# Optimization experiments

Hardware: AMD Instinct MI355X
Metric: run time of the kernel (lower is better)

## Reference

```python
import jax, jax.numpy as jnp
import numpy as np

ANCHOR_PX = (32, 64, 96, 128)
FIELD = 16.0
POOL, TILES = 2, 3
TAU, NMS_IOU = 0.5, 0.3
MAX_DET = 512
HF, WF, DF = 128, 128, 512
HIDDEN = 1024


def _create_anchors():
    # anchors centered on the field grid, rows ordered (i, j, k): x,y = upper-left, w=h=size
    ii, jj, kk = np.meshgrid(np.arange(HF), np.arange(WF), np.arange(len(ANCHOR_PX)), indexing='ij')
    sz = np.asarray(ANCHOR_PX, np.float32)[kk]
    x = jj * FIELD + FIELD / 2 - sz / 2
    y = ii * FIELD + FIELD / 2 - sz / 2
    return np.stack([x.ravel(), y.ravel(), sz.ravel(), sz.ravel()], axis=1).astype(np.float32)


def setup_inputs() -> dict:
    key = jax.random.key(0)
    ks = jax.random.split(key, 8)
    return {
        'features': jax.random.normal(ks[0], (HF, WF, DF), jnp.float32),
        'rpn_obj': jax.random.normal(ks[1], (HF, WF, 2 * len(ANCHOR_PX)), jnp.float32),
        'rpn_reg': 0.1 * jax.random.normal(ks[2], (HF, WF, 4 * len(ANCHOR_PX)), jnp.float32),
        'anchors': jnp.asarray(_create_anchors()),
        'W1': 0.02 * jax.random.normal(ks[3], (TILES * TILES * DF, HIDDEN), jnp.float32),
        'b1': jnp.zeros((HIDDEN,), jnp.float32),
        'W2': 0.02 * jax.random.normal(ks[4], (HIDDEN, HIDDEN), jnp.float32),
        'b2': jnp.zeros((HIDDEN,), jnp.float32),
        'W3': 0.02 * jax.random.normal(ks[5], (HIDDEN, 4), jnp.float32),
        'b3': jnp.zeros((4,), jnp.float32),
    }


def _map_outputs(output, anchors):
    # faithful port of map_outputs: 3D RPN tensor -> per-anchor rows via gather
    K = len(ANCHOR_PX)
    ap = jnp.asarray(ANCHOR_PX, jnp.float32)
    idx = jnp.argmax(anchors[:, 3:4] == ap[None, :], axis=1).astype(jnp.int32)
    px = ((anchors[:, 0] + anchors[:, 2] / 2) / FIELD).astype(jnp.int32)
    py = ((anchors[:, 1] + anchors[:, 3] / 2) / FIELD).astype(jnp.int32)
    H, W, D = output.shape
    reshaped = output.reshape(H, W, K, D // K)
    return reshaped[py, px, idx]  # (Na, D//K)


def _unparameterize(reg, anchors):
    acx = anchors[:, 0] + anchors[:, 2] / 2
    acy = anchors[:, 1] + anchors[:, 3] / 2
    cx = acx + reg[:, 0] * anchors[:, 2]
    cy = acy + reg[:, 1] * anchors[:, 3]
    w = anchors[:, 2] * jnp.exp(reg[:, 2])
    h = anchors[:, 3] * jnp.exp(reg[:, 3])
    return jnp.stack([cx - w / 2, cy - h / 2, w, h], axis=1)


def _iou_matrix(boxes):
    x1, y1 = boxes[:, 0], boxes[:, 1]
    x2, y2 = x1 + boxes[:, 2], y1 + boxes[:, 3]
    ix = jnp.maximum(0.0, jnp.minimum(x2[:, None], x2[None, :]) - jnp.maximum(x1[:, None], x1[None, :]))
    iy = jnp.maximum(0.0, jnp.minimum(y2[:, None], y2[None, :]) - jnp.maximum(y1[:, None], y1[None, :]))
    inter = ix * iy
    area = boxes[:, 2] * boxes[:, 3]
    return inter / (area[:, None] + area[None, :] - inter + 1e-8)


def _nms_keep(iou, valid, thr):
    # greedy NMS on score-sorted boxes: sequential scan over rows
    n = valid.shape[0]
    rng = jnp.arange(n)
    def step(keep, i):
        suppressed = jnp.any((iou[i] > thr) & keep & (rng < i))
        k = valid[i] & jnp.logical_not(suppressed)
        return keep.at[i].set(k), k
    keep, _ = jax.lax.scan(step, jnp.zeros((n,), bool), rng)
    return keep


def _roialign(features, boxes):
    # pool x pool bilinear samples per tile, tiles x tiles tiles per box, max-pooled per tile
    M = boxes.shape[0]
    T = TILES * POOL
    t = (jnp.arange(T, dtype=jnp.float32) + 0.5) / T
    fx = (boxes[:, 0:1] + t[None, :] * boxes[:, 2:3]) / FIELD - 0.5  # (M, T)
    fy = (boxes[:, 1:2] + t[None, :] * boxes[:, 3:4]) / FIELD - 0.5
    def grid(c, n):
        c = jnp.clip(c, 0.0, n - 1.0)
        c0 = jnp.floor(c).astype(jnp.int32)
        c1 = jnp.minimum(c0 + 1, n - 1)
        return c0, c1, c - c0
    x0, x1, wx = grid(fx, WF)
    y0, y1, wy = grid(fy, HF)
    def g(yi, xi):
        return features[yi[:, :, None], xi[:, None, :]]  # (M, T, T, D)
    wy0, wy1 = (1 - wy)[:, :, None, None], wy[:, :, None, None]
    wx0, wx1 = (1 - wx)[:, None, :, None], wx[:, None, :, None]
    val = g(y0, x0) * wy0 * wx0 + g(y0, x1) * wy0 * wx1 + g(y1, x0) * wy1 * wx0 + g(y1, x1) * wy1 * wx1
    val = val.reshape(M, TILES, POOL, TILES, POOL, DF)
    return jnp.max(val, axis=(2, 4))  # (M, TILES, TILES, D)


def reference(features, rpn_obj, rpn_reg, anchors, W1, b1, W2, b2, W3, b3):
    obj = _map_outputs(rpn_obj, anchors)            # (Na, 2)
    reg = _map_outputs(rpn_reg, anchors)            # (Na, 4)
    scores = jax.nn.softmax(obj, axis=1)[:, 1]      # objectness
    boxes = _unparameterize(reg, anchors)           # proposals (Na, 4)
    # threshold + top-k (fixed-shape surrogate for boolean_mask)
    masked = jnp.where(scores > TAU, scores, -jnp.inf)
    top_scores, top_idx = jax.lax.top_k(masked, MAX_DET)
    valid = jnp.isfinite(top_scores)
    sel = boxes[top_idx]                            # (MAX_DET, 4)
    keep = _nms_keep(_iou_matrix(sel), valid, NMS_IOU)
    # roialign + fast-rcnn refinement head
    pooled = _roialign(features, sel).reshape(MAX_DET, -1)
    h = jax.nn.relu(pooled @ W1 + b1)
    h = jax.nn.relu(h @ W2 + b2)
    deltas = h @ W3 + b3
    refined = _unparameterize(deltas, sel)
    sc = jnp.where(valid, top_scores, 0.0)
    out = jnp.concatenate([refined, sc[:, None]], axis=1)
    return out * keep[:, None].astype(out.dtype)    # (MAX_DET, 5)
```

## Files before the change

kernel.cpp:

```cpp
#include <hip/hip_runtime.h>
#include <math.h>

#define HFD 128
#define WFD 128
#define DFD 512
#define KA  4
#define NA  (HFD*WFD*KA)
#define MAXD 512
#define HID 1024
#define FIN 4608
#define CMAX 2048
#define NBUCK 1025
#define BINCAP 64
#define TAUF 0.5f
#define NMS_THR 0.3f
#define SPLITK 8

typedef __bf16 bf16x8 __attribute__((ext_vector_type(8)));
typedef float  floatx4 __attribute__((ext_vector_type(4)));

__device__ __forceinline__ unsigned short f2bf(float x) {
    unsigned u = __float_as_uint(x);
    unsigned r = (u + 0x7FFFu + ((u >> 16) & 1u)) >> 16;
    return (unsigned short)r;
}

__global__ void init_kernel(unsigned* __restrict__ hist) {
    int t = threadIdx.x;
    for (int i = t; i < NBUCK; i += 1024) hist[i] = 0u;
}

__global__ __launch_bounds__(256)
void front_kernel(const float* __restrict__ rpn_obj,
                  unsigned* __restrict__ hist,
                  unsigned long long* __restrict__ bins,
                  const float* __restrict__ W1,
                  unsigned short* __restrict__ W1t,
                  const float* __restrict__ W2,
                  unsigned short* __restrict__ W2t) {
    __shared__ float tile[32][33];
    int b = blockIdx.x;
    if (b < 256) {
        int n = b * 256 + threadIdx.x;
        float2 o = ((const float2*)rpn_obj)[n];
        float m  = fmaxf(o.x, o.y);
        float e0 = expf(o.x - m), e1 = expf(o.y - m);
        float s  = e1 / (e0 + e1);
        if (s > TAUF) {
            unsigned bits = __float_as_uint(s);
            unsigned bk = (bits - 0x3F000000u) >> 13;
            unsigned slot = atomicAdd(&hist[bk], 1u);
            if (slot < BINCAP)
                bins[bk * BINCAP + slot] =
                    ((unsigned long long)bits << 32) |
                    (unsigned long long)(~(unsigned)n);
        }
        return;
    }
    b -= 256;
    const float* W; unsigned short* Wt; int K, N;
    if (b < (FIN / 32) * (HID / 32)) { W = W1; Wt = W1t; K = FIN; N = HID; }
    else { b -= (FIN / 32) * (HID / 32); W = W2; Wt = W2t; K = HID; N = HID; }
    int bn = (b & (N / 32 - 1)) * 32;
    int bk = (b / (N / 32)) * 32;
    int tx = threadIdx.x & 31, ty = threadIdx.x >> 5;
#pragma unroll
    for (int r = 0; r < 32; r += 8)
        tile[ty + r][tx] = W[(long)(bk + ty + r) * N + bn + tx];
    __syncthreads();
#pragma unroll
    for (int r = 0; r < 32; r += 8)
        Wt[(long)(bn + ty + r) * K + bk + tx] = f2bf(tile[tx][ty + r]);
}

__global__ __launch_bounds__(1024)
void tgs_kernel(const unsigned* __restrict__ hist,
                const unsigned long long* __restrict__ bins,
                const float* __restrict__ rpn_reg,
                const float* __restrict__ anchors,
                float* __restrict__ sel,
                float* __restrict__ top_score,
                unsigned* __restrict__ valid_g) {
    __shared__ unsigned long long keys[CMAX];
    __shared__ unsigned Hs[NBUCK];
    __shared__ unsigned Ssc[1024];
    __shared__ unsigned cntS;
    __shared__ unsigned thrS;

    int tid = threadIdx.x;
    int wave = tid >> 6, lane = tid & 63;

    if (tid == 0) cntS = 0u;
    for (int i = tid; i < NBUCK; i += 1024) Hs[i] = hist[i];
    __syncthreads();
    unsigned sv = Hs[tid + 1];
    Ssc[tid] = sv;
    __syncthreads();
    for (int d = 1; d < 1024; d <<= 1) {
        unsigned add = (tid + d < 1024) ? Ssc[tid + d] : 0u;
        __syncthreads();
        Ssc[tid] += add;
        __syncthreads();
    }
    if (tid == 0 && Ssc[0] < MAXD) thrS = 0u;
    {
        unsigned Scur = Ssc[tid];
        unsigned Snxt = (tid == 1023) ? 0u : Ssc[tid + 1];
        if (Scur >= MAXD && Snxt < MAXD) thrS = (unsigned)(tid + 1);
    }
    __syncthreads();
    unsigned thr = thrS;

    for (int b = (int)thr + wave; b < NBUCK; b += 16) {
        unsigned c = Hs[b]; if (c > BINCAP) c = BINCAP;
        unsigned base = 0;
        if (lane == 0 && c > 0) base = atomicAdd(&cntS, c);
        base = __shfl(base, 0);
        if (c > 0 && lane < c && base + lane < CMAX)
            keys[base + lane] = bins[(long)b * BINCAP + lane];
    }
    __syncthreads();
    unsigned cnt = cntS; if (cnt > CMAX) cnt = CMAX;
    int SN = (cnt <= 1024) ? 1024 : CMAX;
    for (int i = tid; i < SN; i += 1024)
        if (i >= (int)cnt) keys[i] = 0ULL;
    __syncthreads();

    for (int k = 2; k <= SN; k <<= 1) {
        for (int j = k >> 1; j > 0; j >>= 1) {
            for (int i = tid; i < SN; i += 1024) {
                int ixj = i ^ j;
                if (ixj > i) {
                    unsigned long long a = keys[i], b = keys[ixj];
                    bool up = ((i & k) == 0);
                    if ((a < b) == up) { keys[i] = b; keys[ixj] = a; }
                }
            }
            __syncthreads();
        }
    }

    if (tid < MAXD) {
        unsigned long long e = keys[tid];
        unsigned sbits = (unsigned)(e >> 32);
        bool v = (sbits != 0u);
        unsigned idx = v ? (unsigned)(~(unsigned)e) : 0u;
        int cell = idx >> 2, kk = idx & 3;
        float4 rg = *(const float4*)&rpn_reg[cell * 16 + 4 * kk];
        float4 an = *(const float4*)&anchors[idx * 4];
        float acx = an.x + an.z * 0.5f;
        float acy = an.y + an.w * 0.5f;
        float cx = acx + rg.x * an.z;
        float cy = acy + rg.y * an.w;
        float w  = an.z * expf(rg.z);
        float h  = an.w * expf(rg.w);
        ((float4*)sel)[tid] = make_float4(cx - 0.5f * w, cy - 0.5f * h, w, h);
        top_score[tid] = v ? __uint_as_float(sbits) : 0.0f;
        valid_g[tid]   = v ? 1u : 0u;
    }
}

__global__ __launch_bounds__(512)
void iou_mask_kernel(const float* __restrict__ sel,
                     unsigned long long* __restrict__ mask) {
    int i = blockIdx.x;
    int j = threadIdx.x;
    float4 bi = ((const float4*)sel)[i];
    float4 bj = ((const float4*)sel)[j];
    float x2i = bi.x + bi.z, y2i = bi.y + bi.w;
    float x2j = bj.x + bj.z, y2j = bj.y + bj.w;
    float ai = bi.z * bi.w, aj = bj.z * bj.w;
    float ix = fmaxf(0.0f, fminf(x2i, x2j) - fmaxf(bi.x, bj.x));
    float iy = fmaxf(0.0f, fminf(y2i, y2j) - fmaxf(bi.y, bj.y));
    float inter = ix * iy;
    float iou = inter / (ai + aj - inter + 1e-8f);
    unsigned long long bal = __ballot(iou > NMS_THR);
    if ((j & 63) == 0) mask[i * 8 + (j >> 6)] = bal;
}

__global__ __launch_bounds__(64)
void nms_scan_kernel(const unsigned long long* __restrict__ mask,
                     const unsigned* __restrict__ valid,
                     unsigned* __restrict__ keep) {
    int lane = threadIdx.x;
    unsigned long long w[8][8];
#pragma unroll
    for (int g = 0; g < 8; ++g)
#pragma unroll
        for (int t = 0; t < 8; ++t)
            if (t <= g) w[g][t] = mask[(g * 64 + lane) * 8 + t];
    unsigned long long vb[8];
#pragma unroll
    for (int g = 0; g < 8; ++g)
        vb[g] = __ballot(valid[g * 64 + lane] != 0u);

    unsigned long long keepw[8];
#pragma unroll
    for (int g = 0; g < 8; ++g) {
        bool pre = false;
#pragma unroll
        for (int t = 0; t < 8; ++t)
            if (t < g) pre = pre || ((w[g][t] & keepw[t]) != 0ULL);
        unsigned long long alive = vb[g] & ~__ballot(pre);
        unsigned long long intra = w[g][g];
        unsigned long long kg = 0ULL;
#pragma unroll
        for (int b = 0; b < 64; ++b) {
            unsigned long long sup = __ballot((intra >> b) & 1ULL);
            if ((alive >> b) & 1ULL) {
                kg |= 1ULL << b;
                alive &= ~sup;
            }
        }
        keepw[g] = kg;
        keep[g * 64 + lane] = (unsigned)((kg >> lane) & 1ULL);
    }
}

__global__ __launch_bounds__(256)
void roialign_kernel(const float* __restrict__ feat,
                     const float* __restrict__ sel,
                     unsigned short* __restrict__ pooled) {
    int mrow = blockIdx.x;
    int c = threadIdx.x;
    float4 b = ((const float4*)sel)[mrow];
    float bx = b.x, by = b.y, bw = b.z, bh = b.w;
    float vmax0[9], vmax1[9];
#pragma unroll
    for (int t = 0; t < 9; ++t) { vmax0[t] = -INFINITY; vmax1[t] = -INFINITY; }
#pragma unroll
    for (int p = 0; p < 6; ++p) {
        float fy = (by + ((float)p + 0.5f) / 6.0f * bh) / 16.0f - 0.5f;
        fy = fminf(fmaxf(fy, 0.0f), 127.0f);
        int y0 = (int)floorf(fy);
        int y1 = min(y0 + 1, 127);
        float wy = fy - (float)y0;
#pragma unroll
        for (int q = 0; q < 6; ++q) {
            float fx = (bx + ((float)q + 0.5f) / 6.0f * bw) / 16.0f - 0.5f;
            fx = fminf(fmaxf(fx, 0.0f), 127.0f);
            int x0 = (int)floorf(fx);
            int x1 = min(x0 + 1, 127);
            float wx = fx - (float)x0;
            const float* f00 = feat + (y0 * WFD + x0) * DFD;
            const float* f01 = feat + (y0 * WFD + x1) * DFD;
            const float* f10 = feat + (y1 * WFD + x0) * DFD;
            const float* f11 = feat + (y1 * WFD + x1) * DFD;
            float w00 = (1.0f - wy) * (1.0f - wx);
            float w01 = (1.0f - wy) * wx;
            float w10 = wy * (1.0f - wx);
            float w11 = wy * wx;
            int t = (p >> 1) * 3 + (q >> 1);
            float v0 = f00[c] * w00 + f01[c] * w01 + f10[c] * w10 + f11[c] * w11;
            float v1 = f00[c + 256] * w00 + f01[c + 256] * w01 +
                       f10[c + 256] * w10 + f11[c + 256] * w11;
            vmax0[t] = fmaxf(vmax0[t], v0);
            vmax1[t] = fmaxf(vmax1[t], v1);
        }
    }
#pragma unroll
    for (int t = 0; t < 9; ++t) {
        pooled[mrow * FIN + t * DFD + c] = f2bf(vmax0[t]);
        pooled[mrow * FIN + t * DFD + c + 256] = f2bf(vmax1[t]);
    }
}

#define LDSTRIDE 40
__global__ __launch_bounds__(256)
void mfma_gemm_kernel(const unsigned short* __restrict__ A,
                      const unsigned short* __restrict__ Bt,
                      float* __restrict__ Cpart,
                      int M, int N, int K) {
    __shared__ unsigned short As[64 * LDSTRIDE];
    __shared__ unsigned short Bs[64 * LDSTRIDE];
    int tid = threadIdx.x;
    int wave = tid >> 6, lane = tid & 63;
    int bm = blockIdx.y * 64, bn = blockIdx.x * 64;
    int KC = K / SPLITK;
    int ks = blockIdx.z * KC;

    floatx4 acc[4] = {};
    int lr = tid >> 2;
    int lk = (tid & 3) << 3;
    int frow = lane & 15, quad = lane >> 4;

    const unsigned short* Ap = A + (long)(bm + lr) * K + lk;
    const unsigned short* Bp = Bt + (long)(bn + lr) * K + lk;

    for (int k0 = ks; k0 < ks + KC; k0 += 32) {
        uint4 av = *(const uint4*)(Ap + k0);
        uint4 bv = *(const uint4*)(Bp + k0);
        *(uint4*)&As[lr * LDSTRIDE + lk] = av;
        *(uint4*)&Bs[lr * LDSTRIDE + lk] = bv;
        __syncthreads();
        bf16x8 af = *(const bf16x8*)&As[(wave * 16 + frow) * LDSTRIDE + quad * 8];
#pragma unroll
        for (int t = 0; t < 4; ++t) {
            bf16x8 bfv = *(const bf16x8*)&Bs[(t * 16 + frow) * LDSTRIDE + quad * 8];
            acc[t] = __builtin_amdgcn_mfma_f32_16x16x32_bf16(af, bfv, acc[t], 0, 0, 0);
        }
        __syncthreads();
    }

    float* Cp = Cpart + (long)blockIdx.z * M * N;
#pragma unroll
    for (int t = 0; t < 4; ++t) {
#pragma unroll
        for (int r = 0; r < 4; ++r) {
            int m = bm + wave * 16 + quad * 4 + r;
            int n = bn + t * 16 + frow;
            Cp[(long)m * N + n] = acc[t][r];
        }
    }
}

__global__ __launch_bounds__(256)
void reduce_bias_relu_kernel(const float* __restrict__ Cpart,
                             const float* __restrict__ bias,
                             unsigned short* __restrict__ out_bf,
                             int MN, int N) {
    int i4 = (blockIdx.x * blockDim.x + threadIdx.x) * 4;
    if (i4 >= MN) return;
    float4 s = *(const float4*)&Cpart[i4];
#pragma unroll
    for (int z = 1; z < SPLITK; ++z) {
        float4 p = *(const float4*)&Cpart[(long)z * MN + i4];
        s.x += p.x; s.y += p.y; s.z += p.z; s.w += p.w;
    }
    int n = i4 & (N - 1);
    float4 bi = *(const float4*)&bias[n];
    s.x = fmaxf(s.x + bi.x, 0.0f);
    s.y = fmaxf(s.y + bi.y, 0.0f);
    s.z = fmaxf(s.z + bi.z, 0.0f);
    s.w = fmaxf(s.w + bi.w, 0.0f);
    uint2 o;
    o.x = (unsigned)f2bf(s.x) | ((unsigned)f2bf(s.y) << 16);
    o.y = (unsigned)f2bf(s.z) | ((unsigned)f2bf(s.w) << 16);
    *(uint2*)&out_bf[i4] = o;
}

__global__ __launch_bounds__(256)
void rowhead_kernel(const float* __restrict__ Cpart,
                    const float* __restrict__ b2,
                    const float* __restrict__ W3,
                    const float* __restrict__ b3,
                    const float* __restrict__ sel,
                    const float* __restrict__ top_score,
                    const unsigned* __restrict__ valid,
                    const unsigned* __restrict__ keep,
                    float* __restrict__ out) {
    __shared__ float red[4][4];
    int r = blockIdx.x, t = threadIdx.x;
    int wave = t >> 6, lane = t & 63;
    int c = t * 4;
    const int MN = MAXD * HID;
    float4 s = *(const float4*)&Cpart[(long)r * HID + c];
#pragma unroll
    for (int z = 1; z < SPLITK; ++z) {
        float4 p = *(const float4*)&Cpart[(long)z * MN + (long)r * HID + c];
        s.x += p.x; s.y += p.y; s.z += p.z; s.w += p.w;
    }
    float4 bi = *(const float4*)&b2[c];
    float h[4];
    h[0] = fmaxf(s.x + bi.x, 0.0f);
    h[1] = fmaxf(s.y + bi.y, 0.0f);
    h[2] = fmaxf(s.z + bi.z, 0.0f);
    h[3] = fmaxf(s.w + bi.w, 0.0f);
    float a0 = 0.f, a1 = 0.f, a2 = 0.f, a3 = 0.f;
#pragma unroll
    for (int i = 0; i < 4; ++i) {
        float4 w = *(const float4*)&W3[(c + i) * 4];
        a0 += h[i] * w.x; a1 += h[i] * w.y;
        a2 += h[i] * w.z; a3 += h[i] * w.w;
    }
#pragma unroll
    for (int off = 32; off > 0; off >>= 1) {
        a0 += __shfl_down(a0, off);
        a1 += __shfl_down(a1, off);
        a2 += __shfl_down(a2, off);
        a3 += __shfl_down(a3, off);
    }
    if (lane == 0) {
        red[wave][0] = a0; red[wave][1] = a1;
        red[wave][2] = a2; red[wave][3] = a3;
    }
    __syncthreads();
    if (t == 0) {
        float d0 = red[0][0] + red[1][0] + red[2][0] + red[3][0] + b3[0];
        float d1 = red[0][1] + red[1][1] + red[2][1] + red[3][1] + b3[1];
        float d2 = red[0][2] + red[1][2] + red[2][2] + red[3][2] + b3[2];
        float d3 = red[0][3] + red[1][3] + red[2][3] + red[3][3] + b3[3];
        if (keep[r] != 0u) {
            float4 b = ((const float4*)sel)[r];
            float acx = b.x + 0.5f * b.z;
            float acy = b.y + 0.5f * b.w;
            float cx = acx + d0 * b.z;
            float cy = acy + d1 * b.w;
            float nw = b.z * expf(d2);
            float nh = b.w * expf(d3);
            out[r * 5 + 0] = cx - 0.5f * nw;
            out[r * 5 + 1] = cy - 0.5f * nh;
            out[r * 5 + 2] = nw;
            out[r * 5 + 3] = nh;
            out[r * 5 + 4] = (valid[r] != 0u) ? top_score[r] : 0.0f;
        } else {
            out[r * 5 + 0] = 0.0f;
            out[r * 5 + 1] = 0.0f;
            out[r * 5 + 2] = 0.0f;
            out[r * 5 + 3] = 0.0f;
            out[r * 5 + 4] = 0.0f;
        }
    }
}

extern "C" void kernel_launch(void* const* d_in, const int* in_sizes, int n_in,
                              void* d_out, int out_size, void* d_ws, size_t ws_size,
                              hipStream_t stream) {
    const float* features = (const float*)d_in[0];
    const float* rpn_obj  = (const float*)d_in[1];
    const float* rpn_reg  = (const float*)d_in[2];
    const float* anchors  = (const float*)d_in[3];
    const float* W1 = (const float*)d_in[4];
    const float* b1 = (const float*)d_in[5];
    const float* W2 = (const float*)d_in[6];
    const float* b2 = (const float*)d_in[7];
    const float* W3 = (const float*)d_in[8];
    const float* b3 = (const float*)d_in[9];
    float* out = (float*)d_out;

    char* ws = (char*)d_ws;
    size_t off = 0;
    auto alloc = [&](size_t bytes) {
        char* p = ws + off;
        off += (bytes + 255) & ~(size_t)255;
        return p;
    };
    unsigned* hist      = (unsigned*)alloc(NBUCK * sizeof(unsigned));
    unsigned long long* bins =
        (unsigned long long*)alloc((size_t)NBUCK * BINCAP * 8);
    float*    sel       = (float*)alloc(MAXD * 4 * sizeof(float));
    float*    top_score = (float*)alloc(MAXD * sizeof(float));
    unsigned* valid     = (unsigned*)alloc(MAXD * sizeof(unsigned));
    unsigned* keep      = (unsigned*)alloc(MAXD * sizeof(unsigned));
    unsigned long long* mask = (unsigned long long*)alloc(MAXD * 8 * 8);
    unsigned short* pooled = (unsigned short*)alloc((size_t)MAXD * FIN * 2);
    unsigned short* W1t = (unsigned short*)alloc((size_t)FIN * HID * 2);
    unsigned short* W2t = (unsigned short*)alloc((size_t)HID * HID * 2);
    unsigned short* h1  = (unsigned short*)alloc((size_t)MAXD * HID * 2);
    float*    Cpart     = (float*)alloc((size_t)SPLITK * MAXD * HID * sizeof(float));
    (void)ws_size; (void)in_sizes; (void)n_in; (void)out_size;

    const int TBLOCKS = (FIN / 32) * (HID / 32) + (HID / 32) * (HID / 32);
    init_kernel<<<1, 1024, 0, stream>>>(hist);
    front_kernel<<<256 + TBLOCKS, 256, 0, stream>>>(rpn_obj, hist, bins,
                                                    W1, W1t, W2, W2t);
    tgs_kernel<<<1, 1024, 0, stream>>>(hist, bins, rpn_reg, anchors,
                                       sel, top_score, valid);
    iou_mask_kernel<<<MAXD, 512, 0, stream>>>(sel, mask);
    nms_scan_kernel<<<1, 64, 0, stream>>>(mask, valid, keep);
    roialign_kernel<<<MAXD, 256, 0, stream>>>(features, sel, pooled);

    const int MN = MAXD * HID;
    mfma_gemm_kernel<<<dim3(HID / 64, MAXD / 64, SPLITK), 256, 0, stream>>>(
        pooled, W1t, Cpart, MAXD, HID, FIN);
    reduce_bias_relu_kernel<<<MN / 4 / 256, 256, 0, stream>>>(
        Cpart, b1, h1, MN, HID);
    mfma_gemm_kernel<<<dim3(HID / 64, MAXD / 64, SPLITK), 256, 0, stream>>>(
        h1, W2t, Cpart, MAXD, HID, HID);
    rowhead_kernel<<<MAXD, 256, 0, stream>>>(Cpart, b2, W3, b3, sel,
                                             top_score, valid, keep, out);
}
```

Measured before the change: 201.7 us.

## Fuse NMS into RoIAlign kernel, widen GEMM K-step, halve split-K

Merges the IoU-mask and NMS-scan kernels into an extra block of the RoIAlign launch, so the whole NMS runs in one block that keeps the mask in shared memory. This removes two launches and the global mask buffer. The GEMM now loads 64 K-elements per iteration with two MFMAs per tile, which halves the number of barriers, and SPLITK drops from 8 to 4 to cut partial-sum traffic. The risk is that the single NMS block computes 512x512 IoUs serially per thread and may become the critical path, and the GEMM grid now has fewer blocks.

```diff
diff --git a/kernel.cpp b/kernel.cpp
--- a/kernel.cpp
+++ b/kernel.cpp
@@ -14,7 +14,7 @@
 #define BINCAP 64
 #define TAUF 0.5f
 #define NMS_THR 0.3f
-#define SPLITK 8
+#define SPLITK 4
 
 typedef __bf16 bf16x8 __attribute__((ext_vector_type(8)));
 typedef float  floatx4 __attribute__((ext_vector_type(4)));
@@ -160,74 +160,76 @@
     }
 }
 
-__global__ __launch_bounds__(512)
-void iou_mask_kernel(const float* __restrict__ sel,
-                     unsigned long long* __restrict__ mask) {
-    int i = blockIdx.x;
-    int j = threadIdx.x;
-    float4 bi = ((const float4*)sel)[i];
-    float4 bj = ((const float4*)sel)[j];
-    float x2i = bi.x + bi.z, y2i = bi.y + bi.w;
-    float x2j = bj.x + bj.z, y2j = bj.y + bj.w;
-    float ai = bi.z * bi.w, aj = bj.z * bj.w;
-    float ix = fmaxf(0.0f, fminf(x2i, x2j) - fmaxf(bi.x, bj.x));
-    float iy = fmaxf(0.0f, fminf(y2i, y2j) - fmaxf(bi.y, bj.y));
-    float inter = ix * iy;
-    float iou = inter / (ai + aj - inter + 1e-8f);
-    unsigned long long bal = __ballot(iou > NMS_THR);
-    if ((j & 63) == 0) mask[i * 8 + (j >> 6)] = bal;
-}
-
-__global__ __launch_bounds__(64)
-void nms_scan_kernel(const unsigned long long* __restrict__ mask,
-                     const unsigned* __restrict__ valid,
-                     unsigned* __restrict__ keep) {
-    int lane = threadIdx.x;
-    unsigned long long w[8][8];
-#pragma unroll
-    for (int g = 0; g < 8; ++g)
-#pragma unroll
-        for (int t = 0; t < 8; ++t)
-            if (t <= g) w[g][t] = mask[(g * 64 + lane) * 8 + t];
-    unsigned long long vb[8];
-#pragma unroll
-    for (int g = 0; g < 8; ++g)
-        vb[g] = __ballot(valid[g * 64 + lane] != 0u);
-
-    unsigned long long keepw[8];
-#pragma unroll
-    for (int g = 0; g < 8; ++g) {
-        bool pre = false;
-#pragma unroll
-        for (int t = 0; t < 8; ++t)
-            if (t < g) pre = pre || ((w[g][t] & keepw[t]) != 0ULL);
-        unsigned long long alive = vb[g] & ~__ballot(pre);
-        unsigned long long intra = w[g][g];
-        unsigned long long kg = 0ULL;
-#pragma unroll
-        for (int b = 0; b < 64; ++b) {
-            unsigned long long sup = __ballot((intra >> b) & 1ULL);
-            if ((alive >> b) & 1ULL) {
-                kg |= 1ULL << b;
-                alive &= ~sup;
+__global__ __launch_bounds__(256)
+void roialign_nms_kernel(const float* __restrict__ feat,
+                         const float* __restrict__ sel,
+                         const unsigned* __restrict__ valid,
+                         unsigned* __restrict__ keep,
+                         unsigned short* __restrict__ pooled) {
+    __shared__ float4 selL[MAXD];
+    __shared__ unsigned long long maskL[MAXD][8];
+    int t = threadIdx.x;
+
+    if (blockIdx.x == 0) {
+        for (int i = t; i < MAXD; i += 256) selL[i] = ((const float4*)sel)[i];
+        __syncthreads();
+        for (int rr = 0; rr < 2; ++rr) {
+            int r = t + rr * 256;
+            float4 bi = selL[r];
+            float x2i = bi.x + bi.z, y2i = bi.y + bi.w;
+            float ai = bi.z * bi.w;
+            for (int w = 0; w < 8; ++w) {
+                unsigned long long mw = 0ULL;
+                for (int b = 0; b < 64; ++b) {
+                    float4 bj = selL[w * 64 + b];
+                    float x2j = bj.x + bj.z, y2j = bj.y + bj.w;
+                    float aj = bj.z * bj.w;
+                    float ix = fmaxf(0.0f, fminf(x2i, x2j) - fmaxf(bi.x, bj.x));
+                    float iy = fmaxf(0.0f, fminf(y2i, y2j) - fmaxf(bi.y, bj.y));
+                    float inter = ix * iy;
+                    float iou = inter / (ai + aj - inter + 1e-8f);
+                    if (iou > NMS_THR) mw |= 1ULL << b;
+                }
+                maskL[r][w] = mw;
             }
         }
-        keepw[g] = kg;
-        keep[g * 64 + lane] = (unsigned)((kg >> lane) & 1ULL);
-    }
-}
-
-__global__ __launch_bounds__(256)
-void roialign_kernel(const float* __restrict__ feat,
-                     const float* __restrict__ sel,
-                     unsigned short* __restrict__ pooled) {
-    int mrow = blockIdx.x;
-    int c = threadIdx.x;
+        __syncthreads();
+        if (t < 64) {
+            int lane = t;
+            unsigned long long keepw[8];
+#pragma unroll
+            for (int g = 0; g < 8; ++g) {
+                bool pre = false;
+#pragma unroll
+                for (int t2 = 0; t2 < 8; ++t2)
+                    if (t2 < g)
+                        pre = pre || ((maskL[g * 64 + lane][t2] & keepw[t2]) != 0ULL);
+                unsigned long long vbg = __ballot(valid[g * 64 + lane] != 0u);
+                unsigned long long alive = vbg & ~__ballot(pre);
+                unsigned long long intra = maskL[g * 64 + lane][g];
+                unsigned long long kg = 0ULL;
+#pragma unroll
+                for (int b = 0; b < 64; ++b) {
+                    unsigned long long sup = __ballot((intra >> b) & 1ULL);
+                    if ((alive >> b) & 1ULL) {
+                        kg |= 1ULL << b;
+                        alive &= ~sup;
+                    }
+                }
+                keepw[g] = kg;
+                keep[g * 64 + lane] = (unsigned)((kg >> lane) & 1ULL);
+            }
+        }
+        return;
+    }
+
+    int mrow = blockIdx.x - 1;
+    int c = t;
     float4 b = ((const float4*)sel)[mrow];
     float bx = b.x, by = b.y, bw = b.z, bh = b.w;
     float vmax0[9], vmax1[9];
 #pragma unroll
-    for (int t = 0; t < 9; ++t) { vmax0[t] = -INFINITY; vmax1[t] = -INFINITY; }
+    for (int tt = 0; tt < 9; ++tt) { vmax0[tt] = -INFINITY; vmax1[tt] = -INFINITY; }
 #pragma unroll
     for (int p = 0; p < 6; ++p) {
         float fy = (by + ((float)p + 0.5f) / 6.0f * bh) / 16.0f - 0.5f;
@@ -250,29 +252,29 @@
             float w01 = (1.0f - wy) * wx;
             float w10 = wy * (1.0f - wx);
             float w11 = wy * wx;
-            int t = (p >> 1) * 3 + (q >> 1);
+            int tt = (p >> 1) * 3 + (q >> 1);
             float v0 = f00[c] * w00 + f01[c] * w01 + f10[c] * w10 + f11[c] * w11;
             float v1 = f00[c + 256] * w00 + f01[c + 256] * w01 +
                        f10[c + 256] * w10 + f11[c + 256] * w11;
-            vmax0[t] = fmaxf(vmax0[t], v0);
-            vmax1[t] = fmaxf(vmax1[t], v1);
-        }
-    }
-#pragma unroll
-    for (int t = 0; t < 9; ++t) {
-        pooled[mrow * FIN + t * DFD + c] = f2bf(vmax0[t]);
-        pooled[mrow * FIN + t * DFD + c + 256] = f2bf(vmax1[t]);
-    }
-}
-
-#define LDSTRIDE 40
+            vmax0[tt] = fmaxf(vmax0[tt], v0);
+            vmax1[tt] = fmaxf(vmax1[tt], v1);
+        }
+    }
+#pragma unroll
+    for (int tt = 0; tt < 9; ++tt) {
+        pooled[mrow * FIN + tt * DFD + c] = f2bf(vmax0[tt]);
+        pooled[mrow * FIN + tt * DFD + c + 256] = f2bf(vmax1[tt]);
+    }
+}
+
+#define LDK 72
 __global__ __launch_bounds__(256)
 void mfma_gemm_kernel(const unsigned short* __restrict__ A,
                       const unsigned short* __restrict__ Bt,
                       float* __restrict__ Cpart,
                       int M, int N, int K) {
-    __shared__ unsigned short As[64 * LDSTRIDE];
-    __shared__ unsigned short Bs[64 * LDSTRIDE];
+    __shared__ unsigned short As[64 * LDK];
+    __shared__ unsigned short Bs[64 * LDK];
     int tid = threadIdx.x;
     int wave = tid >> 6, lane = tid & 63;
     int bm = blockIdx.y * 64, bn = blockIdx.x * 64;
@@ -281,23 +283,30 @@
 
     floatx4 acc[4] = {};
     int lr = tid >> 2;
-    int lk = (tid & 3) << 3;
+    int lk = (tid & 3) << 4;
     int frow = lane & 15, quad = lane >> 4;
 
     const unsigned short* Ap = A + (long)(bm + lr) * K + lk;
     const unsigned short* Bp = Bt + (long)(bn + lr) * K + lk;
 
-    for (int k0 = ks; k0 < ks + KC; k0 += 32) {
-        uint4 av = *(const uint4*)(Ap + k0);
-        uint4 bv = *(const uint4*)(Bp + k0);
-        *(uint4*)&As[lr * LDSTRIDE + lk] = av;
-        *(uint4*)&Bs[lr * LDSTRIDE + lk] = bv;
-        __syncthreads();
-        bf16x8 af = *(const bf16x8*)&As[(wave * 16 + frow) * LDSTRIDE + quad * 8];
+    for (int k0 = ks; k0 < ks + KC; k0 += 64) {
+        uint4 a0 = *(const uint4*)(Ap + k0);
+        uint4 a1 = *(const uint4*)(Ap + k0 + 8);
+        uint4 b0 = *(const uint4*)(Bp + k0);
+        uint4 b1 = *(const uint4*)(Bp + k0 + 8);
+        *(uint4*)&As[lr * LDK + lk] = a0;
+        *(uint4*)&As[lr * LDK + lk + 8] = a1;
+        *(uint4*)&Bs[lr * LDK + lk] = b0;
+        *(uint4*)&Bs[lr * LDK + lk + 8] = b1;
+        __syncthreads();
+        bf16x8 af0 = *(const bf16x8*)&As[(wave * 16 + frow) * LDK + quad * 8];
+        bf16x8 af1 = *(const bf16x8*)&As[(wave * 16 + frow) * LDK + 32 + quad * 8];
 #pragma unroll
         for (int t = 0; t < 4; ++t) {
-            bf16x8 bfv = *(const bf16x8*)&Bs[(t * 16 + frow) * LDSTRIDE + quad * 8];
-            acc[t] = __builtin_amdgcn_mfma_f32_16x16x32_bf16(af, bfv, acc[t], 0, 0, 0);
+            bf16x8 b0v = *(const bf16x8*)&Bs[(t * 16 + frow) * LDK + quad * 8];
+            bf16x8 b1v = *(const bf16x8*)&Bs[(t * 16 + frow) * LDK + 32 + quad * 8];
+            acc[t] = __builtin_amdgcn_mfma_f32_16x16x32_bf16(af0, b0v, acc[t], 0, 0, 0);
+            acc[t] = __builtin_amdgcn_mfma_f32_16x16x32_bf16(af1, b1v, acc[t], 0, 0, 0);
         }
         __syncthreads();
     }
@@ -442,7 +451,6 @@
     float*    top_score = (float*)alloc(MAXD * sizeof(float));
     unsigned* valid     = (unsigned*)alloc(MAXD * sizeof(unsigned));
     unsigned* keep      = (unsigned*)alloc(MAXD * sizeof(unsigned));
-    unsigned long long* mask = (unsigned long long*)alloc(MAXD * 8 * 8);
     unsigned short* pooled = (unsigned short*)alloc((size_t)MAXD * FIN * 2);
     unsigned short* W1t = (unsigned short*)alloc((size_t)FIN * HID * 2);
     unsigned short* W2t = (unsigned short*)alloc((size_t)HID * HID * 2);
@@ -456,9 +464,8 @@
                                                     W1, W1t, W2, W2t);
     tgs_kernel<<<1, 1024, 0, stream>>>(hist, bins, rpn_reg, anchors,
                                        sel, top_score, valid);
-    iou_mask_kernel<<<MAXD, 512, 0, stream>>>(sel, mask);
-    nms_scan_kernel<<<1, 64, 0, stream>>>(mask, valid, keep);
-    roialign_kernel<<<MAXD, 256, 0, stream>>>(features, sel, pooled);
+    roialign_nms_kernel<<<MAXD + 1, 256, 0, stream>>>(features, sel,
+                                                      valid, keep, pooled);
 
     const int MN = MAXD * HID;
     mfma_gemm_kernel<<<dim3(HID / 64, MAXD / 64, SPLITK), 256, 0, stream>>>(
```

New measurement: 272.7 us. +35.2%, slower.

## Split roialign per tile, widen GEMM k-step, halve split-K, memset histogram

Applied to the files above, without the earlier changes.

RoIAlign now launches one block per (ROI, output tile), which multiplies the block count by nine and shrinks per-thread register state. The bf16 MFMA GEMM loads 64-wide K chunks per iteration with a padded LDS stride, halving the barrier count per K step. Split-K drops from 8 to 4, reducing partial-sum writes and reduction traffic at the cost of fewer GEMM blocks. The histogram init kernel is replaced by hipMemsetAsync.

```diff
diff --git a/kernel.cpp b/kernel.cpp
--- a/kernel.cpp
+++ b/kernel.cpp
@@ -14,7 +14,7 @@
 #define BINCAP 64
 #define TAUF 0.5f
 #define NMS_THR 0.3f
-#define SPLITK 8
+#define SPLITK 4
 
 typedef __bf16 bf16x8 __attribute__((ext_vector_type(8)));
 typedef float  floatx4 __attribute__((ext_vector_type(4)));
@@ -23,11 +23,6 @@
     unsigned u = __float_as_uint(x);
     unsigned r = (u + 0x7FFFu + ((u >> 16) & 1u)) >> 16;
     return (unsigned short)r;
-}
-
-__global__ void init_kernel(unsigned* __restrict__ hist) {
-    int t = threadIdx.x;
-    for (int i = t; i < NBUCK; i += 1024) hist[i] = 0u;
 }
 
 __global__ __launch_bounds__(256)
@@ -221,23 +216,25 @@
 void roialign_kernel(const float* __restrict__ feat,
                      const float* __restrict__ sel,
                      unsigned short* __restrict__ pooled) {
-    int mrow = blockIdx.x;
+    int blk = blockIdx.x;
+    int mrow = blk / 9;
+    int tile = blk - mrow * 9;
+    int tp = tile / 3, tq = tile - tp * 3;
     int c = threadIdx.x;
     float4 b = ((const float4*)sel)[mrow];
-    float bx = b.x, by = b.y, bw = b.z, bh = b.w;
-    float vmax0[9], vmax1[9];
-#pragma unroll
-    for (int t = 0; t < 9; ++t) { vmax0[t] = -INFINITY; vmax1[t] = -INFINITY; }
-#pragma unroll
-    for (int p = 0; p < 6; ++p) {
-        float fy = (by + ((float)p + 0.5f) / 6.0f * bh) / 16.0f - 0.5f;
+    float vmax0 = -INFINITY, vmax1 = -INFINITY;
+#pragma unroll
+    for (int dp = 0; dp < 2; ++dp) {
+        int p = tp * 2 + dp;
+        float fy = (b.y + ((float)p + 0.5f) / 6.0f * b.w) / 16.0f - 0.5f;
         fy = fminf(fmaxf(fy, 0.0f), 127.0f);
         int y0 = (int)floorf(fy);
         int y1 = min(y0 + 1, 127);
         float wy = fy - (float)y0;
 #pragma unroll
-        for (int q = 0; q < 6; ++q) {
-            float fx = (bx + ((float)q + 0.5f) / 6.0f * bw) / 16.0f - 0.5f;
+        for (int dq = 0; dq < 2; ++dq) {
+            int q = tq * 2 + dq;
+            float fx = (b.x + ((float)q + 0.5f) / 6.0f * b.z) / 16.0f - 0.5f;
             fx = fminf(fmaxf(fx, 0.0f), 127.0f);
             int x0 = (int)floorf(fx);
             int x1 = min(x0 + 1, 127);
@@ -250,29 +247,25 @@
             float w01 = (1.0f - wy) * wx;
             float w10 = wy * (1.0f - wx);
             float w11 = wy * wx;
-            int t = (p >> 1) * 3 + (q >> 1);
             float v0 = f00[c] * w00 + f01[c] * w01 + f10[c] * w10 + f11[c] * w11;
             float v1 = f00[c + 256] * w00 + f01[c + 256] * w01 +
                        f10[c + 256] * w10 + f11[c + 256] * w11;
-            vmax0[t] = fmaxf(vmax0[t], v0);
-            vmax1[t] = fmaxf(vmax1[t], v1);
-        }
-    }
-#pragma unroll
-    for (int t = 0; t < 9; ++t) {
-        pooled[mrow * FIN + t * DFD + c] = f2bf(vmax0[t]);
-        pooled[mrow * FIN + t * DFD + c + 256] = f2bf(vmax1[t]);
-    }
-}
-
-#define LDSTRIDE 40
+            vmax0 = fmaxf(vmax0, v0);
+            vmax1 = fmaxf(vmax1, v1);
+        }
+    }
+    pooled[mrow * FIN + tile * DFD + c] = f2bf(vmax0);
+    pooled[mrow * FIN + tile * DFD + c + 256] = f2bf(vmax1);
+}
+
+#define LDK 72
 __global__ __launch_bounds__(256)
 void mfma_gemm_kernel(const unsigned short* __restrict__ A,
                       const unsigned short* __restrict__ Bt,
                       float* __restrict__ Cpart,
                       int M, int N, int K) {
-    __shared__ unsigned short As[64 * LDSTRIDE];
-    __shared__ unsigned short Bs[64 * LDSTRIDE];
+    __shared__ unsigned short As[64 * LDK];
+    __shared__ unsigned short Bs[64 * LDK];
     int tid = threadIdx.x;
     int wave = tid >> 6, lane = tid & 63;
     int bm = blockIdx.y * 64, bn = blockIdx.x * 64;
@@ -281,23 +274,30 @@
 
     floatx4 acc[4] = {};
     int lr = tid >> 2;
-    int lk = (tid & 3) << 3;
+    int lk = (tid & 3) << 4;
     int frow = lane & 15, quad = lane >> 4;
 
     const unsigned short* Ap = A + (long)(bm + lr) * K + lk;
     const unsigned short* Bp = Bt + (long)(bn + lr) * K + lk;
 
-    for (int k0 = ks; k0 < ks + KC; k0 += 32) {
-        uint4 av = *(const uint4*)(Ap + k0);
-        uint4 bv = *(const uint4*)(Bp + k0);
-        *(uint4*)&As[lr * LDSTRIDE + lk] = av;
-        *(uint4*)&Bs[lr * LDSTRIDE + lk] = bv;
+    for (int k0 = ks; k0 < ks + KC; k0 += 64) {
+        uint4 a0 = *(const uint4*)(Ap + k0);
+        uint4 a1 = *(const uint4*)(Ap + k0 + 8);
+        uint4 b0 = *(const uint4*)(Bp + k0);
+        uint4 b1 = *(const uint4*)(Bp + k0 + 8);
+        *(uint4*)&As[lr * LDK + lk] = a0;
+        *(uint4*)&As[lr * LDK + lk + 8] = a1;
+        *(uint4*)&Bs[lr * LDK + lk] = b0;
+        *(uint4*)&Bs[lr * LDK + lk + 8] = b1;
         __syncthreads();
-        bf16x8 af = *(const bf16x8*)&As[(wave * 16 + frow) * LDSTRIDE + quad * 8];
+        bf16x8 af0 = *(const bf16x8*)&As[(wave * 16 + frow) * LDK + quad * 8];
+        bf16x8 af1 = *(const bf16x8*)&As[(wave * 16 + frow) * LDK + 32 + quad * 8];
 #pragma unroll
         for (int t = 0; t < 4; ++t) {
-            bf16x8 bfv = *(const bf16x8*)&Bs[(t * 16 + frow) * LDSTRIDE + quad * 8];
-            acc[t] = __builtin_amdgcn_mfma_f32_16x16x32_bf16(af, bfv, acc[t], 0, 0, 0);
+            bf16x8 b0v = *(const bf16x8*)&Bs[(t * 16 + frow) * LDK + quad * 8];
+            bf16x8 b1v = *(const bf16x8*)&Bs[(t * 16 + frow) * LDK + 32 + quad * 8];
+            acc[t] = __builtin_amdgcn_mfma_f32_16x16x32_bf16(af0, b0v, acc[t], 0, 0, 0);
+            acc[t] = __builtin_amdgcn_mfma_f32_16x16x32_bf16(af1, b1v, acc[t], 0, 0, 0);
         }
         __syncthreads();
     }
@@ -451,14 +451,14 @@
     (void)ws_size; (void)in_sizes; (void)n_in; (void)out_size;
 
     const int TBLOCKS = (FIN / 32) * (HID / 32) + (HID / 32) * (HID / 32);
-    init_kernel<<<1, 1024, 0, stream>>>(hist);
+    hipMemsetAsync(hist, 0, NBUCK * sizeof(unsigned), stream);
     front_kernel<<<256 + TBLOCKS, 256, 0, stream>>>(rpn_obj, hist, bins,
                                                     W1, W1t, W2, W2t);
     tgs_kernel<<<1, 1024, 0, stream>>>(hist, bins, rpn_reg, anchors,
                                        sel, top_score, valid);
     iou_mask_kernel<<<MAXD, 512, 0, stream>>>(sel, mask);
     nms_scan_kernel<<<1, 64, 0, stream>>>(mask, valid, keep);
-    roialign_kernel<<<MAXD, 256, 0, stream>>>(features, sel, pooled);
+    roialign_kernel<<<MAXD * 9, 256, 0, stream>>>(features, sel, pooled);
 
     const int MN = MAXD * HID;
     mfma_gemm_kernel<<<dim3(HID / 64, MAXD / 64, SPLITK), 256, 0, stream>>>(
```

Measured after the change: 195.6 us. 1.03x faster.
